# Kernel optimization log

Measured on AMD Instinct MI355X. Metric: run time of the kernel, lower is better.

The kernel has to match this reference:

```python
import jax, jax.numpy as jnp
import numpy as np

B, T, C = 2, 2048, 2048
N_HEAD = 16
HD = C // N_HEAD  # 128


def setup_inputs() -> dict:
    key = jax.random.key(0)
    k1, k2, k3, k4, k5 = jax.random.split(key, 5)
    s_in = 1.0 / np.sqrt(C)
    return {
        "x": jax.random.normal(k1, (B, T, C), dtype=jnp.float32),
        # weights stored as (in, out), i.e. transpose of torch Linear weight
        "W_attn": jax.random.normal(k2, (C, 3 * C), dtype=jnp.float32) * s_in,
        "b_attn": jax.random.normal(k3, (3 * C,), dtype=jnp.float32) * 0.02,
        "W_proj": jax.random.normal(k4, (C, C), dtype=jnp.float32) * s_in,
        "b_proj": jax.random.normal(k5, (C,), dtype=jnp.float32) * 0.02,
    }


def reference(x, W_attn, b_attn, W_proj, b_proj):
    # qkv projection: (B,T,3C)
    qkv = x @ W_attn + b_attn
    q, k, v = jnp.split(qkv, 3, axis=-1)
    # (B, n_head, T, head_dim)
    q = q.reshape(B, T, N_HEAD, HD).transpose(0, 2, 1, 3)
    k = k.reshape(B, T, N_HEAD, HD).transpose(0, 2, 1, 3)
    v = v.reshape(B, T, N_HEAD, HD).transpose(0, 2, 1, 3)
    # scores (B,H,T,T), causal mask (T_q == T_k prefill path)
    att = jnp.einsum("bhqd,bhkd->bhqk", q, k) * (1.0 / np.sqrt(HD))
    causal = jnp.tril(jnp.ones((T, T), dtype=bool))
    att = jnp.where(causal[None, None], att, -jnp.inf)
    att = jax.nn.softmax(att, axis=-1)  # attn_dropout is identity (p=0)
    y = jnp.einsum("bhqk,bhkd->bhqd", att, v)
    y = y.transpose(0, 2, 1, 3).reshape(B, T, C)
    y = y @ W_proj + b_proj  # resid_dropout identity (p=0)
    # new_cache = (k, v, T) since T == block_size; return output tensor
    return y
```

## Files before the change

kernel.cpp:

```cpp
#include <hip/hip_runtime.h>
#include <cstdint>
#include <cstddef>


typedef __bf16 bf16x8 __attribute__((ext_vector_type(8)));
typedef float  f32x4  __attribute__((ext_vector_type(4)));
typedef unsigned short u16x4 __attribute__((ext_vector_type(4)));
typedef unsigned short u16x8 __attribute__((ext_vector_type(8)));

__device__ __forceinline__ unsigned short f2bf(float f) {
  unsigned int u = __builtin_bit_cast(unsigned int, f);
  u += 0x7fffu + ((u >> 16) & 1u);
  return (unsigned short)(u >> 16);
}

__device__ __forceinline__ void gld16(void* lds, const void* g) {
  __builtin_amdgcn_global_load_lds(
      (const __attribute__((address_space(1))) void*)g,
      (__attribute__((address_space(3))) void*)lds, 16, 0, 0);
}

__global__ void cvt_f32_bf16_k(const float* __restrict__ in,
                               unsigned short* __restrict__ out, int n4) {
  int i = blockIdx.x * blockDim.x + threadIdx.x;
  int stride = gridDim.x * blockDim.x;
  for (; i < n4; i += stride) {
    float4 v = ((const float4*)in)[i];
    ushort4 o;
    o.x = f2bf(v.x); o.y = f2bf(v.y); o.z = f2bf(v.z); o.w = f2bf(v.w);
    ((ushort4*)out)[i] = o;
  }
}

__global__ __launch_bounds__(256) void transpose_f32_bf16(
    const float* __restrict__ in, unsigned short* __restrict__ out,
    int R, int C) {
  __shared__ float tile[64][65];
  int c0 = blockIdx.x * 64, r0 = blockIdx.y * 64;
  int t = threadIdx.x;
  int lr = t >> 4, lc = (t & 15) * 4;
#pragma unroll
  for (int i = 0; i < 4; i++) {
    int row = lr + i * 16;
    float4 v = *(const float4*)&in[(size_t)(r0 + row) * C + c0 + lc];
    tile[row][lc] = v.x; tile[row][lc + 1] = v.y;
    tile[row][lc + 2] = v.z; tile[row][lc + 3] = v.w;
  }
  __syncthreads();
  int wr = t >> 3, wc = (t & 7) * 8;
#pragma unroll
  for (int i = 0; i < 2; i++) {
    int crow = wr + i * 32;
    u16x8 o;
#pragma unroll
    for (int j = 0; j < 8; j++) o[j] = f2bf(tile[wc + j][crow]);
    *(u16x8*)&out[(size_t)(c0 + crow) * R + r0 + wc] = o;
  }
}

__global__ __launch_bounds__(256) void extract_vT_k(
    const unsigned short* __restrict__ qkv, unsigned short* __restrict__ vT) {
  __shared__ unsigned int tile32[64][33];
  int bh = blockIdx.z, b = bh >> 4, h = bh & 15;
  int t0 = blockIdx.x * 64, d0 = blockIdx.y * 64;
  int t = threadIdx.x;
  int lr = t >> 3, lc = (t & 7) * 8;
  const unsigned short* src = qkv + (size_t)(b * 2048) * 6144 + 4096 + h * 128;
#pragma unroll
  for (int i = 0; i < 2; i++) {
    int row = lr + i * 32;
    u16x8 v = *(const u16x8*)&src[(size_t)(t0 + row) * 6144 + d0 + lc];
#pragma unroll
    for (int j = 0; j < 8; j++) {
      unsigned short* p = (unsigned short*)&tile32[lc + j][row & 31];
      p[row >> 5] = v[j];
    }
  }
  __syncthreads();
  int dr = t >> 2, tc = (t & 3) * 8;
  u16x8 lo, hi;
#pragma unroll
  for (int j = 0; j < 8; j++) {
    unsigned int u = tile32[dr][tc + j];
    lo[j] = (unsigned short)(u & 0xffffu);
    hi[j] = (unsigned short)(u >> 16);
  }
  unsigned short* dst = vT + (size_t)bh * 128 * 2048 + (size_t)(d0 + dr) * 2048 + t0;
  *(u16x8*)&dst[tc] = lo;
  *(u16x8*)&dst[tc + 32] = hi;
}

template <int OUT_BF16>
__global__ __launch_bounds__(256) void gemm_bt(
    const unsigned short* __restrict__ A, const unsigned short* __restrict__ BT,
    const float* __restrict__ bias, void* __restrict__ Cout,
    int M, int N, int K) {
  __shared__ __align__(16) unsigned short sA[128 * 64];
  __shared__ __align__(16) unsigned short sB[128 * 64];

  const int tid = threadIdx.x, w = tid >> 6, lane = tid & 63;
  const int quad = lane >> 4, l16 = lane & 15;
  const int m0 = blockIdx.y * 128, n0 = blockIdx.x * 128;
  const int wr = w >> 1, wc = w & 1;

  const unsigned short* gA[4];
  const unsigned short* gB[4];
  unsigned short* lA[4];
  unsigned short* lB[4];
#pragma unroll
  for (int i = 0; i < 4; i++) {
    int c = w * 256 + i * 64 + lane;
    int row = c >> 3, scol = (c & 7) ^ (row & 7);
    gA[i] = A + (size_t)(m0 + row) * K + scol * 8;
    gB[i] = BT + (size_t)(n0 + row) * K + scol * 8;
    lA[i] = sA + (size_t)(w * 256 + i * 64) * 8;
    lB[i] = sB + (size_t)(w * 256 + i * 64) * 8;
  }

  f32x4 acc[4][4] = {};

  for (int k0 = 0; k0 < K; k0 += 64) {
#pragma unroll
    for (int i = 0; i < 4; i++) {
      gld16(lA[i], gA[i]); gld16(lB[i], gB[i]);
      gA[i] += 64; gB[i] += 64;
    }
    __syncthreads();

#pragma unroll
    for (int kk = 0; kk < 2; kk++) {
      const int cc = (kk * 4 + quad) ^ (l16 & 7);
      bf16x8 af[4], bfr[4];
#pragma unroll
      for (int mi = 0; mi < 4; mi++)
        af[mi] = *(const bf16x8*)&sA[(wr * 64 + mi * 16 + l16) * 64 + cc * 8];
#pragma unroll
      for (int ni = 0; ni < 4; ni++)
        bfr[ni] = *(const bf16x8*)&sB[(wc * 64 + ni * 16 + l16) * 64 + cc * 8];
#pragma unroll
      for (int mi = 0; mi < 4; mi++)
#pragma unroll
        for (int ni = 0; ni < 4; ni++)
          acc[mi][ni] = __builtin_amdgcn_mfma_f32_16x16x32_bf16(
              af[mi], bfr[ni], acc[mi][ni], 0, 0, 0);
    }
    __syncthreads();
  }

#pragma unroll
  for (int mi = 0; mi < 4; mi++) {
    int row = m0 + wr * 64 + mi * 16 + quad * 4;
#pragma unroll
    for (int ni = 0; ni < 4; ni++) {
      int col = n0 + wc * 64 + ni * 16 + l16;
      float bv = bias[col];
#pragma unroll
      for (int r = 0; r < 4; r++) {
        float v = acc[mi][ni][r] + bv;
        if (OUT_BF16)
          ((unsigned short*)Cout)[(size_t)(row + r) * N + col] = f2bf(v);
        else
          ((float*)Cout)[(size_t)(row + r) * N + col] = v;
      }
    }
  }
}

__global__ __launch_bounds__(256) void flash_attn(
    const unsigned short* __restrict__ qkv, const unsigned short* __restrict__ vT,
    unsigned short* __restrict__ yout) {
  __shared__ __align__(16) unsigned short sK[2][64 * 128];
  __shared__ __align__(16) unsigned short sVT[2][128 * 64];
  __shared__ __align__(16) unsigned short sP[4 * 16 * 64];

  const int tid = threadIdx.x, w = tid >> 6, lane = tid & 63;
  const int quad = lane >> 4, l16 = lane & 15;
  const int id = blockIdx.x;
  const int g = id & 31;
  const int qp = id >> 5;
  const int b = g >> 4, h = g & 15;
  const int T = 2048, CC = 6144, HD = 128;
  const float qscale = 0.12753257252f;

  const unsigned short* gK = qkv + (size_t)(b * T) * CC + 2048 + h * HD;
  const unsigned short* gV = vT + (size_t)(b * 16 + h) * HD * T;
  unsigned short* pw = sP + w * 16 * 64;

  const unsigned short* kSrc[4];
  const unsigned short* vSrc[4];
  unsigned short* kDst[4];
  unsigned short* vDst[4];
#pragma unroll
  for (int i = 0; i < 4; i++) {
    int c = w * 256 + i * 64 + lane;
    int kR = c >> 4, kC = (c & 15) ^ (kR & 15);
    int vR = c >> 3, vC = (c & 7) ^ (vR & 7);
    kSrc[i] = gK + (size_t)kR * CC + kC * 8;
    vSrc[i] = gV + (size_t)vR * T + vC * 8;
    kDst[i] = (unsigned short*)sK + (size_t)(w * 256 + i * 64) * 8;
    vDst[i] = (unsigned short*)sVT + (size_t)(w * 256 + i * 64) * 8;
  }
  const int KBUF = 64 * 128, VBUF = 128 * 64;

  const int qtA = qp, qtB = 31 - qp;
  int qt = qtA, kt = 0;

  bf16x8 qf[4];
  float m_old, l_sum;
  f32x4 o[8] = {};
  {
    const size_t qrow = (size_t)(b * T + qt * 64 + w * 16 + l16) * CC + h * HD;
#pragma unroll
    for (int kb = 0; kb < 4; kb++) {
      bf16x8 raw = *(const bf16x8*)&qkv[qrow + kb * 32 + quad * 8];
      bf16x8 sc;
#pragma unroll
      for (int j = 0; j < 8; j++) sc[j] = (__bf16)((float)raw[j] * qscale);
      qf[kb] = sc;
    }
  }
  m_old = -1e30f; l_sum = 0.f;

#pragma unroll
  for (int i = 0; i < 4; i++) {
    gld16(kDst[i], kSrc[i]);
    gld16(vDst[i], vSrc[i]);
  }

  const int total = qtA + qtB + 2;
  for (int it = 0; it < total; ++it) {
    __syncthreads();
    const int cur = it & 1;
    const bool segEnd = (kt == qt);

    if (it + 1 < total) {
      const int nkt = segEnd ? 0 : kt + 1;
      const int nb_ = (it + 1) & 1;
      const size_t kOff = (size_t)nkt * 64 * CC;
      const int vOff = nkt * 64;
#pragma unroll
      for (int i = 0; i < 4; i++) {
        gld16(kDst[i] + (size_t)nb_ * KBUF, kSrc[i] + kOff);
        gld16(vDst[i] + (size_t)nb_ * VBUF, vSrc[i] + vOff);
      }
    }

    const unsigned short* sKc = (const unsigned short*)sK + (size_t)cur * KBUF;
    const unsigned short* sVc = (const unsigned short*)sVT + (size_t)cur * VBUF;

    f32x4 s4[4] = {};
#pragma unroll
    for (int dc = 0; dc < 4; dc++) {
#pragma unroll
      for (int kb = 0; kb < 4; kb++) {
        int rr = kb * 16 + l16;
        int cc = (dc * 4 + quad) ^ l16;
        bf16x8 kf = *(const bf16x8*)&sKc[rr * 128 + cc * 8];
        s4[kb] = __builtin_amdgcn_mfma_f32_16x16x32_bf16(kf, qf[dc], s4[kb], 0, 0, 0);
      }
    }

    float sv[4][4];
#pragma unroll
    for (int kb = 0; kb < 4; kb++)
#pragma unroll
      for (int r = 0; r < 4; r++) {
        float v = s4[kb][r];
        if (segEnd) {
          if (kb * 16 + quad * 4 + r > w * 16 + l16) v = -1e30f;
        }
        sv[kb][r] = v;
      }

    float mx = sv[0][0];
#pragma unroll
    for (int kb = 0; kb < 4; kb++)
#pragma unroll
      for (int r = 0; r < 4; r++) mx = fmaxf(mx, sv[kb][r]);
    mx = fmaxf(mx, __shfl_xor(mx, 16));
    mx = fmaxf(mx, __shfl_xor(mx, 32));
    float m_new = fmaxf(m_old, mx);
    float a = exp2f(m_old - m_new);
    float ssum = 0.f;
#pragma unroll
    for (int kb = 0; kb < 4; kb++)
#pragma unroll
      for (int r = 0; r < 4; r++) {
        float p = exp2f(sv[kb][r] - m_new);
        sv[kb][r] = p;
        ssum += p;
      }
    ssum += __shfl_xor(ssum, 16);
    ssum += __shfl_xor(ssum, 32);
    l_sum = l_sum * a + ssum;
    m_old = m_new;

    float ar[4];
#pragma unroll
    for (int r = 0; r < 4; r++)
      ar[r] = __shfl(a, (lane & 48) + quad * 4 + r);
#pragma unroll
    for (int nb = 0; nb < 8; nb++)
#pragma unroll
      for (int r = 0; r < 4; r++) o[nb][r] *= ar[r];

#pragma unroll
    for (int kb = 0; kb < 4; kb++) {
      u16x4 pk;
#pragma unroll
      for (int r = 0; r < 4; r++) pk[r] = f2bf(sv[kb][r]);
      int c = kb * 2 + (quad >> 1);
      int cp = c ^ (l16 & 7);
      *(u16x4*)&pw[l16 * 64 + cp * 8 + (quad & 1) * 4] = pk;
    }

#pragma unroll
    for (int kb2 = 0; kb2 < 2; kb2++) {
      int pcc = (kb2 * 4 + quad) ^ (l16 & 7);
      bf16x8 pf = *(const bf16x8*)&pw[l16 * 64 + pcc * 8];
#pragma unroll
      for (int nb = 0; nb < 8; nb++) {
        int rr = nb * 16 + l16;
        int cc = (kb2 * 4 + quad) ^ (rr & 7);
        bf16x8 vf = *(const bf16x8*)&sVc[rr * 64 + cc * 8];
        o[nb] = __builtin_amdgcn_mfma_f32_16x16x32_bf16(pf, vf, o[nb], 0, 0, 0);
      }
    }

    if (segEnd) {
      float linv = 1.0f / l_sum;
#pragma unroll
      for (int r = 0; r < 4; r++) {
        float ir = __shfl(linv, (lane & 48) + quad * 4 + r);
        size_t orow = (size_t)(b * T + qt * 64 + w * 16 + quad * 4 + r) * 2048 + h * HD;
#pragma unroll
        for (int nb = 0; nb < 8; nb++)
          yout[orow + nb * 16 + l16] = f2bf(o[nb][r] * ir);
      }
      if (it + 1 < total) {
        qt = qtB;
        const size_t qrow = (size_t)(b * T + qt * 64 + w * 16 + l16) * CC + h * HD;
#pragma unroll
        for (int kb = 0; kb < 4; kb++) {
          bf16x8 raw = *(const bf16x8*)&qkv[qrow + kb * 32 + quad * 8];
          bf16x8 sc;
#pragma unroll
          for (int j = 0; j < 8; j++) sc[j] = (__bf16)((float)raw[j] * qscale);
          qf[kb] = sc;
        }
        m_old = -1e30f; l_sum = 0.f;
#pragma unroll
        for (int nb = 0; nb < 8; nb++) o[nb] = (f32x4){0.f, 0.f, 0.f, 0.f};
      }
      kt = 0;
    } else {
      kt++;
    }
  }
}

extern "C" void kernel_launch(void* const* d_in, const int* in_sizes, int n_in,
                              void* d_out, int out_size, void* d_ws, size_t ws_size,
                              hipStream_t stream) {
  const float* x      = (const float*)d_in[0];
  const float* W_attn = (const float*)d_in[1];
  const float* b_attn = (const float*)d_in[2];
  const float* W_proj = (const float*)d_in[3];
  const float* b_proj = (const float*)d_in[4];
  float* out = (float*)d_out;

  char* ws = (char*)d_ws;
  unsigned short* x_bf  = (unsigned short*)(ws);
  unsigned short* WaT   = (unsigned short*)(ws + 16777216);
  unsigned short* WpT   = (unsigned short*)(ws + 41943040);
  unsigned short* qkv   = (unsigned short*)(ws + 50331648);
  unsigned short* vT    = (unsigned short*)(ws + 100663296);
  unsigned short* y_att = (unsigned short*)(ws + 117440512);

  cvt_f32_bf16_k<<<1024, 256, 0, stream>>>(x, x_bf, 8388608 / 4);
  transpose_f32_bf16<<<dim3(96, 32), 256, 0, stream>>>(W_attn, WaT, 2048, 6144);
  transpose_f32_bf16<<<dim3(32, 32), 256, 0, stream>>>(W_proj, WpT, 2048, 2048);
  gemm_bt<1><<<dim3(48, 32), 256, 0, stream>>>(x_bf, WaT, b_attn, qkv, 4096, 6144, 2048);
  extract_vT_k<<<dim3(32, 2, 32), 256, 0, stream>>>(qkv, vT);
  flash_attn<<<dim3(512), 256, 0, stream>>>(qkv, vT, y_att);
  gemm_bt<0><<<dim3(16, 32), 256, 0, stream>>>(y_att, WpT, b_proj, out, 4096, 2048, 2048);
}
```

Measured before the change: 386.2 us.

## Add 256x256 eight-wave GEMM with XCD swizzle for QKV projection

```diff
diff --git a/kernel.cpp b/kernel.cpp
--- a/kernel.cpp
+++ b/kernel.cpp
@@ -166,6 +166,163 @@
   }
 }
 
+#define BARRIER8 __builtin_amdgcn_s_barrier()
+#define WAIT_LGKM0 asm volatile("s_waitcnt lgkmcnt(0)" ::: "memory")
+#define WAIT_VM2 asm volatile("s_waitcnt vmcnt(2)" ::: "memory")
+#define WAIT_VM0 asm volatile("s_waitcnt vmcnt(0)" ::: "memory")
+
+#define STAGE_A(buf, h, t)                                                   \
+  do {                                                                       \
+    gld16(&sA[buf][((h) * 1024 + w * 64) * 8],                               \
+          gA0 + (size_t)(h) * 128 * K + (size_t)(t) * 64);                   \
+    gld16(&sA[buf][((h) * 1024 + 512 + w * 64) * 8],                         \
+          gA1 + (size_t)(h) * 128 * K + (size_t)(t) * 64);                   \
+  } while (0)
+
+#define STAGE_B(buf, h, t)                                                   \
+  do {                                                                       \
+    gld16(&sB[buf][((h) * 1024 + w * 64) * 8],                               \
+          gB0 + (size_t)(h) * 128 * K + (size_t)(t) * 64);                   \
+    gld16(&sB[buf][((h) * 1024 + 512 + w * 64) * 8],                         \
+          gB1 + (size_t)(h) * 128 * K + (size_t)(t) * 64);                   \
+  } while (0)
+
+#define LDA4(buf, mh, kk)                                                    \
+  do {                                                                       \
+    const int cc_ = ((kk) * 4 + quad) ^ (l16 & 7);                           \
+    _Pragma("unroll") for (int i_ = 0; i_ < 4; ++i_) {                       \
+      const int rr_ = wr * 128 + (mh) * 64 + i_ * 16 + l16;                  \
+      a_[i_] = *(const bf16x8*)&sA[buf][rr_ * 64 + cc_ * 8];                 \
+    }                                                                        \
+  } while (0)
+
+#define LDB4(buf, kk)                                                        \
+  do {                                                                       \
+    const int cc_ = ((kk) * 4 + quad) ^ (l16 & 7);                           \
+    _Pragma("unroll") for (int i_ = 0; i_ < 4; ++i_) {                       \
+      const int rr_ = wc * 64 + i_ * 16 + l16;                               \
+      b_[i_] = *(const bf16x8*)&sB[buf][rr_ * 64 + cc_ * 8];                 \
+    }                                                                        \
+  } while (0)
+
+#define MM16(mh)                                                             \
+  do {                                                                       \
+    __builtin_amdgcn_s_setprio(1);                                           \
+    _Pragma("unroll") for (int i_ = 0; i_ < 4; ++i_)                         \
+    _Pragma("unroll") for (int n_ = 0; n_ < 4; ++n_)                         \
+        acc[(mh) * 4 + i_][n_] = __builtin_amdgcn_mfma_f32_16x16x32_bf16(    \
+            a_[i_], b_[n_], acc[(mh) * 4 + i_][n_], 0, 0, 0);                \
+    __builtin_amdgcn_s_setprio(0);                                           \
+  } while (0)
+
+template <int OUT_BF16>
+__global__ __launch_bounds__(512, 2) void gemm_bt8(
+    const unsigned short* __restrict__ A, const unsigned short* __restrict__ BT,
+    const float* __restrict__ bias, void* __restrict__ Cout,
+    int M, int N, int K) {
+  __shared__ __align__(16) unsigned short sA[2][256 * 64];
+  __shared__ __align__(16) unsigned short sB[2][256 * 64];
+  (void)M;
+
+  const int tid = threadIdx.x, w = tid >> 6, lane = tid & 63;
+  const int quad = lane >> 4, l16 = lane & 15;
+  const int wr = w >> 2, wc = w & 3;
+
+  const int nwgx = gridDim.x;
+  const int nwg = nwgx * gridDim.y;
+  const int wg = blockIdx.y * nwgx + blockIdx.x;
+  const int q8 = nwg >> 3, r8 = nwg & 7;
+  const int xcd = wg & 7, loc = wg >> 3;
+  const int swz =
+      (xcd < r8 ? xcd * (q8 + 1) : r8 * (q8 + 1) + (xcd - r8) * q8) + loc;
+  const int m0 = (swz / nwgx) * 256;
+  const int n0 = (swz % nwgx) * 256;
+
+  const int c0 = tid, c1 = tid + 512;
+  const int r0c = c0 >> 3, s0c = (c0 & 7) ^ (r0c & 7);
+  const int r1c = c1 >> 3, s1c = (c1 & 7) ^ (r1c & 7);
+  const unsigned short* gA0 = A + (size_t)(m0 + r0c) * K + s0c * 8;
+  const unsigned short* gA1 = A + (size_t)(m0 + r1c) * K + s1c * 8;
+  const unsigned short* gB0 = BT + (size_t)(n0 + r0c) * K + s0c * 8;
+  const unsigned short* gB1 = BT + (size_t)(n0 + r1c) * K + s1c * 8;
+
+  f32x4 acc[8][4] = {};
+  bf16x8 a_[4], b_[4];
+
+  const int NT = K >> 6;
+  const int NI = NT >> 1;
+
+  STAGE_B(0, 0, 0); STAGE_B(0, 1, 0);
+  STAGE_A(0, 0, 0); STAGE_A(0, 1, 0);
+  STAGE_B(1, 0, 1);
+  WAIT_VM2;
+  BARRIER8;
+
+  for (int i = 0; i < NI; ++i) {
+    const int t1 = 2 * i + 1;
+    const int tn0 = 2 * i + 2, tn1 = 2 * i + 3;
+    const bool last = (i == NI - 1);
+
+    LDB4(0, 0); LDA4(0, 0, 0);
+    STAGE_B(1, 1, t1);
+    BARRIER8; WAIT_LGKM0; MM16(0); BARRIER8;
+
+    LDA4(0, 1, 0);
+    STAGE_A(1, 0, t1);
+    BARRIER8; WAIT_LGKM0; MM16(1); BARRIER8;
+
+    LDB4(0, 1); LDA4(0, 0, 1);
+    STAGE_A(1, 1, t1);
+    BARRIER8; WAIT_LGKM0; MM16(0); BARRIER8;
+
+    LDA4(0, 1, 1);
+    if (!last) STAGE_B(0, 0, tn0);
+    if (last) { WAIT_VM0; } else { WAIT_VM2; }
+    BARRIER8; WAIT_LGKM0; MM16(1); BARRIER8;
+
+    LDB4(1, 0); LDA4(1, 0, 0);
+    if (!last) STAGE_B(0, 1, tn0);
+    BARRIER8; WAIT_LGKM0; MM16(0); BARRIER8;
+
+    LDA4(1, 1, 0);
+    if (!last) STAGE_A(0, 0, tn0);
+    BARRIER8; WAIT_LGKM0; MM16(1); BARRIER8;
+
+    LDB4(1, 1); LDA4(1, 0, 1);
+    if (!last) STAGE_A(0, 1, tn0);
+    BARRIER8; WAIT_LGKM0; MM16(0); BARRIER8;
+
+    LDA4(1, 1, 1);
+    if (!last) STAGE_B(1, 0, tn1);
+    if (!last) { WAIT_VM2; }
+    BARRIER8; WAIT_LGKM0; MM16(1); BARRIER8;
+  }
+
+#pragma unroll
+  for (int mi = 0; mi < 8; ++mi) {
+    int row = m0 + wr * 128 + mi * 16 + quad * 4;
+#pragma unroll
+    for (int ni = 0; ni < 4; ++ni) {
+      int col = n0 + wc * 64 + ni * 16 + l16;
+      float bv = bias[col];
+#pragma unroll
+      for (int rr = 0; rr < 4; ++rr) {
+        float v = acc[mi][ni][rr] + bv;
+        if (OUT_BF16)
+          ((unsigned short*)Cout)[(size_t)(row + rr) * N + col] = f2bf(v);
+        else
+          ((float*)Cout)[(size_t)(row + rr) * N + col] = v;
+      }
+    }
+  }
+}
+
+#undef STAGE_A
+#undef STAGE_B
+#undef LDA4
+#undef LDB4
+#undef MM16
+
 __global__ __launch_bounds__(256) void flash_attn(
     const unsigned short* __restrict__ qkv, const unsigned short* __restrict__ vT,
     unsigned short* __restrict__ yout) {
@@ -380,7 +537,7 @@
   cvt_f32_bf16_k<<<1024, 256, 0, stream>>>(x, x_bf, 8388608 / 4);
   transpose_f32_bf16<<<dim3(96, 32), 256, 0, stream>>>(W_attn, WaT, 2048, 6144);
   transpose_f32_bf16<<<dim3(32, 32), 256, 0, stream>>>(W_proj, WpT, 2048, 2048);
-  gemm_bt<1><<<dim3(48, 32), 256, 0, stream>>>(x_bf, WaT, b_attn, qkv, 4096, 6144, 2048);
+  gemm_bt8<1><<<dim3(24, 16), 512, 0, stream>>>(x_bf, WaT, b_attn, qkv, 4096, 6144, 2048);
   extract_vT_k<<<dim3(32, 2, 32), 256, 0, stream>>>(qkv, vT);
   flash_attn<<<dim3(512), 256, 0, stream>>>(qkv, vT, y_att);
   gemm_bt<0><<<dim3(16, 32), 256, 0, stream>>>(y_att, WpT, b_proj, out, 4096, 2048, 2048);
```

Result: slower. 422.9 us (+9.5%).
